# Kernel optimization log

Measured on AMD Instinct MI355X. Metric: run time of the kernel, lower is better.

## Reference

```python
import jax, jax.numpy as jnp
import numpy as np

OUT_FEATURES = 11008
IN_FEATURES = 4096
GROUP_SIZE = 32
NUM_GROUPS = OUT_FEATURES * IN_FEATURES // GROUP_SIZE        # 1,409,024
NUM_PACKED = NUM_GROUPS * (GROUP_SIZE // 8 * 3)              # 16,908,288 bytes


def block_dequantize_3bit(weight_q3, weight_norm):
    """Unpack 3-bit codes (8 values per 3 bytes) and dequantize to fp32."""
    p = weight_q3.reshape(-1, 3).astype(jnp.int32)  # [N/8, 3] bytes
    b0, b1, b2 = p[:, 0], p[:, 1], p[:, 2]
    q = jnp.stack([
        b0 & 7,
        (b0 >> 3) & 7,
        ((b0 >> 6) & 3) | ((b1 & 1) << 2),
        (b1 >> 1) & 7,
        (b1 >> 4) & 7,
        ((b1 >> 7) & 1) | ((b2 & 3) << 1),
        (b2 >> 2) & 7,
        (b2 >> 5) & 7,
    ], axis=-1)                                     # [N/8, 8] codes in 0..7
    q = q.reshape(NUM_GROUPS, GROUP_SIZE).astype(jnp.float32)
    norm = weight_norm.astype(jnp.float32)[:, None]  # [num_groups, 1]
    w = (q / 7.0) * 2.0 * norm - norm                # map [0,7] -> [-norm, norm]
    return w.reshape(OUT_FEATURES, IN_FEATURES)


def setup_inputs() -> dict:
    key = jax.random.key(0)
    k1, k2, k3, k4 = jax.random.split(key, 4)
    x = jax.random.normal(k1, (4, 128, IN_FEATURES), dtype=jnp.float32)
    weight_q3 = jax.random.randint(k2, (NUM_PACKED,), 0, 256, dtype=jnp.int32)
    weight_norm = (jax.random.uniform(k3, (NUM_GROUPS,), dtype=jnp.float32) * 0.1 + 0.01).astype(jnp.float16)
    bias = jax.random.normal(k4, (OUT_FEATURES,), dtype=jnp.float32) * 0.02
    return {"x": x, "weight_q3": weight_q3, "weight_norm": weight_norm, "bias": bias}


def reference(x, weight_q3, weight_norm, bias):
    w = block_dequantize_3bit(weight_q3, weight_norm)  # [out, in] fp32
    return jnp.einsum('bsd,od->bso', x, w) + bias
```

## Files before the change

kernel.cpp:

```cpp
#include <hip/hip_runtime.h>
#include <hip/hip_fp16.h>

#define M_TOTAL 512
#define N_TOTAL 11008
#define K_TOTAL 4096
#define BM 128
#define BN 64
#define BK 64
#define NT (K_TOTAL / BK)
#define LDK 72

typedef short bf16x8 __attribute__((ext_vector_type(8)));
typedef float f32x4 __attribute__((ext_vector_type(4)));

__device__ __forceinline__ unsigned int pack2_bf16(float f0, float f1) {
    unsigned int u0 = __builtin_bit_cast(unsigned int, f0) + 0x8000u;
    unsigned int u1 = __builtin_bit_cast(unsigned int, f1) + 0x8000u;
    return (u0 >> 16) | (u1 & 0xFFFF0000u);
}

__device__ __forceinline__ void async_ld16(void* lds, const void* g) {
    __builtin_amdgcn_global_load_lds(
        (const __attribute__((address_space(1))) unsigned int*)g,
        (__attribute__((address_space(3))) unsigned int*)lds, 16, 0, 0);
}

__device__ __forceinline__ int detect_mode_wave(const void* __restrict__ wn) {
    const int lane = threadIdx.x & 63;
    const unsigned short* u16 = (const unsigned short*)wn;
    const float* f32p = (const float*)wn;
    const float vb = __builtin_bit_cast(float, (unsigned int)u16[lane] << 16);
    const float vh = __half2float(__builtin_bit_cast(__half, u16[lane]));
    const float vf = f32p[lane];
    const unsigned long long mb = __ballot(vb > 0.005f && vb < 0.12f);
    const unsigned long long mh = __ballot(vh > 0.005f && vh < 0.12f);
    (void)vf;
    return (mb == ~0ull) ? 2 : ((mh == ~0ull) ? 1 : 0);
}

__global__ void __launch_bounds__(256)
convert_x_kernel(const float* __restrict__ x, unsigned short* __restrict__ xb) {
    const int i = (blockIdx.x * 256 + threadIdx.x) * 4;
    const float4 v = *(const float4*)&x[i];
    *(uint2*)&xb[i] = make_uint2(pack2_bf16(v.x, v.y), pack2_bf16(v.z, v.w));
}

__global__ void __launch_bounds__(512, 6)
l3b_gemm_pipe(const unsigned short* __restrict__ xb, const int* __restrict__ wq,
              const void* __restrict__ wnorm, const float* __restrict__ bias,
              float* __restrict__ out)
{
    __shared__ unsigned short As[2][BM * 64];
    __shared__ unsigned short Bs[2][BN * 64];

    const int tid  = threadIdx.x;
    const int mode = detect_mode_wave(wnorm);

    const int bid = blockIdx.x;
    const int w   = (bid & 7) * 86 + (bid >> 3);
    const int m0  = (w & 3) * BM;
    const int n0  = (w >> 2) * BN;

    const int wid  = tid >> 6;
    const int lane = tid & 63;
    const int quad = lane >> 4;
    const int lm   = lane & 15;
    const int wm   = (wid >> 1) * 32;
    const int wn_  = (wid & 1) * 32;

    const int arow0 = wid * 8 + (lane >> 3);
    const int acol  = ((lane & 7) ^ ((lane >> 3) & 7)) * 8;
    const int aslot = (lane & 7) * 8;

    const int gl   = tid >> 2;
    const int sub  = tid & 3;
    const int bn_l = gl >> 1;
    const int kg   = gl & 1;
    const int ldsB = (bn_l << 6) + ((((kg * 4 + sub)) ^ (bn_l & 7)) << 3);

    auto stageA = [&](int it, int buf) {
#pragma unroll
        for (int j = 0; j < 2; ++j) {
            const int row = arow0 + j * 64;
            async_ld16(&As[buf][(row << 6) + aslot],
                       &xb[(size_t)(m0 + row) * K_TOTAL + it * 64 + acol]);
        }
    };

    auto loadNorm = [&](int g) -> float {
        if (mode == 0)      return ((const float*)wnorm)[g];
        else if (mode == 1) return __half2float(((const __half*)wnorm)[g]);
        else                return __builtin_bit_cast(float,
                               (unsigned int)((const unsigned short*)wnorm)[g] << 16);
    };
    auto loadB = [&](int it, int& b0, int& b1, int& b2, float& nrm) {
        const int g    = (n0 + bn_l) * (K_TOTAL / 32) + it * 2 + kg;
        const int base = g * 12 + sub * 3;
        b0 = wq[base]; b1 = wq[base + 1]; b2 = wq[base + 2];
        nrm = loadNorm(g);
    };
    auto decodeB = [&](int b0, int b1, int b2, float nrm, int buf) {
        const float a = nrm * (2.0f / 7.0f);
        const float b = -nrm;
        const unsigned int bits =
            (unsigned)b0 | ((unsigned)b1 << 8) | ((unsigned)b2 << 16);
        unsigned int packs[4];
#pragma unroll
        for (int j = 0; j < 4; ++j) {
            const float f0 = fmaf((float)((bits >> (6 * j)) & 7), a, b);
            const float f1 = fmaf((float)((bits >> (6 * j + 3)) & 7), a, b);
            packs[j] = pack2_bf16(f0, f1);
        }
        *(uint4*)&Bs[buf][ldsB] = make_uint4(packs[0], packs[1], packs[2], packs[3]);
    };

    f32x4 acc[2][2];
#pragma unroll
    for (int i = 0; i < 2; ++i)
#pragma unroll
        for (int j = 0; j < 2; ++j) acc[i][j] = (f32x4){0.f, 0.f, 0.f, 0.f};

    auto mfmaTile = [&](const unsigned short* Asb, const unsigned short* Bsb) {
#pragma unroll
        for (int ks = 0; ks < 2; ++ks) {
            const int cswz = (((ks * 4 + quad) ^ (lm & 7)) << 3);
            bf16x8 aF[2], bF[2];
#pragma unroll
            for (int mi = 0; mi < 2; ++mi)
                aF[mi] = *(const bf16x8*)&Asb[((wm + mi * 16 + lm) << 6) + cswz];
#pragma unroll
            for (int ni = 0; ni < 2; ++ni)
                bF[ni] = *(const bf16x8*)&Bsb[((wn_ + ni * 16 + lm) << 6) + cswz];
#pragma unroll
            for (int mi = 0; mi < 2; ++mi)
#pragma unroll
                for (int ni = 0; ni < 2; ++ni)
                    acc[mi][ni] = __builtin_amdgcn_mfma_f32_16x16x32_bf16(
                        aF[mi], bF[ni], acc[mi][ni], 0, 0, 0);
        }
    };

    int b0a, b1a, b2a; float na;
    int b0b, b1b, b2b; float nb;

    stageA(0, 0);
    loadB(0, b0a, b1a, b2a, na);
    decodeB(b0a, b1a, b2a, na, 0);
    loadB(1, b0b, b1b, b2b, nb);
    __syncthreads();

    for (int it = 0; it < NT; it += 2) {
        if (it + 1 < NT) stageA(it + 1, 1);
        if (it + 2 < NT) loadB(it + 2, b0a, b1a, b2a, na);
        if (it + 1 < NT) decodeB(b0b, b1b, b2b, nb, 1);
        mfmaTile(As[0], Bs[0]);
        __syncthreads();

        if (it + 2 < NT) stageA(it + 2, 0);
        if (it + 3 < NT) loadB(it + 3, b0b, b1b, b2b, nb);
        if (it + 2 < NT) decodeB(b0a, b1a, b2a, na, 0);
        mfmaTile(As[1], Bs[1]);
        __syncthreads();
    }

#pragma unroll
    for (int ni = 0; ni < 2; ++ni) {
        const int o  = n0 + wn_ + ni * 16 + lm;
        const float bv = bias[o];
#pragma unroll
        for (int mi = 0; mi < 2; ++mi) {
#pragma unroll
            for (int r = 0; r < 4; ++r) {
                const int m = m0 + wm + mi * 16 + quad * 4 + r;
                out[m * N_TOTAL + o] = acc[mi][ni][r] + bv;
            }
        }
    }
}

__global__ void __launch_bounds__(256)
l3b_gemm_kernel(const float* __restrict__ x, const int* __restrict__ wq,
                const void* __restrict__ wnorm, const float* __restrict__ bias,
                float* __restrict__ out)
{
    __shared__ unsigned short As[128 * LDK];
    __shared__ unsigned short Bs[64 * LDK];

    const int mode = detect_mode_wave(wnorm);
    const int tid  = threadIdx.x;
    const int m0   = blockIdx.y * 128;
    const int n0   = blockIdx.x * 64;
    const int wid  = tid >> 6;
    const int lane = tid & 63;
    const int quad = lane >> 4;
    const int lm   = lane & 15;
    const int wm   = (wid >> 1) * 64;
    const int wn   = (wid & 1) * 32;

    f32x4 acc[4][2];
#pragma unroll
    for (int i = 0; i < 4; ++i)
#pragma unroll
        for (int j = 0; j < 2; ++j) acc[i][j] = (f32x4){0.f, 0.f, 0.f, 0.f};

    const int ar = tid >> 4;
    const int ac = (tid & 15) * 4;
    const int gin      = tid >> 1;
    const int half     = tid & 1;
    const int bn_local = gin >> 1;
    const int bkg      = gin & 1;

    for (int it = 0; it < NT; ++it) {
        const int k0 = it * BK;
        __syncthreads();
#pragma unroll
        for (int p = 0; p < 8; ++p) {
            const int row = p * 16 + ar;
            const float4 v = *(const float4*)&x[(m0 + row) * K_TOTAL + k0 + ac];
            *(uint2*)&As[row * LDK + ac] =
                make_uint2(pack2_bf16(v.x, v.y), pack2_bf16(v.z, v.w));
        }
        {
            const int g    = (n0 + bn_local) * (K_TOTAL / 32) + it * 2 + bkg;
            const int base = g * 12 + half * 6;
            const int2 w0 = *(const int2*)&wq[base];
            const int2 w1 = *(const int2*)&wq[base + 2];
            const int2 w2 = *(const int2*)&wq[base + 4];
            float nrm;
            if (mode == 0)      nrm = ((const float*)wnorm)[g];
            else if (mode == 1) nrm = __half2float(((const __half*)wnorm)[g]);
            else                nrm = __builtin_bit_cast(float,
                                    (unsigned int)((const unsigned short*)wnorm)[g] << 16);
            const float a = nrm * (2.0f / 7.0f);
            const float b = -nrm;
            const unsigned int bits0 =
                (unsigned)w0.x | ((unsigned)w0.y << 8) | ((unsigned)w1.x << 16);
            const unsigned int bits1 =
                (unsigned)w1.y | ((unsigned)w2.x << 8) | ((unsigned)w2.y << 16);
            unsigned int packs[8];
#pragma unroll
            for (int t3 = 0; t3 < 2; ++t3) {
                const unsigned int bits = t3 ? bits1 : bits0;
#pragma unroll
                for (int j = 0; j < 4; ++j) {
                    const float f0 = fmaf((float)((bits >> (6 * j)) & 7), a, b);
                    const float f1 = fmaf((float)((bits >> (6 * j + 3)) & 7), a, b);
                    packs[t3 * 4 + j] = pack2_bf16(f0, f1);
                }
            }
            unsigned int* dst = (unsigned int*)&Bs[bn_local * LDK + bkg * 32 + half * 16];
            *(uint4*)dst       = make_uint4(packs[0], packs[1], packs[2], packs[3]);
            *(uint4*)(dst + 4) = make_uint4(packs[4], packs[5], packs[6], packs[7]);
        }
        __syncthreads();
#pragma unroll
        for (int ks = 0; ks < 2; ++ks) {
            const int kb = ks * 32 + quad * 8;
            bf16x8 aF[4], bF[2];
#pragma unroll
            for (int mi = 0; mi < 4; ++mi)
                aF[mi] = *(const bf16x8*)&As[(wm + mi * 16 + lm) * LDK + kb];
#pragma unroll
            for (int ni = 0; ni < 2; ++ni)
                bF[ni] = *(const bf16x8*)&Bs[(wn + ni * 16 + lm) * LDK + kb];
#pragma unroll
            for (int mi = 0; mi < 4; ++mi)
#pragma unroll
                for (int ni = 0; ni < 2; ++ni)
                    acc[mi][ni] = __builtin_amdgcn_mfma_f32_16x16x32_bf16(
                        aF[mi], bF[ni], acc[mi][ni], 0, 0, 0);
        }
    }
#pragma unroll
    for (int ni = 0; ni < 2; ++ni) {
        const int o  = n0 + wn + ni * 16 + lm;
        const float bv = bias[o];
#pragma unroll
        for (int mi = 0; mi < 4; ++mi)
#pragma unroll
            for (int r = 0; r < 4; ++r) {
                const int m = m0 + wm + mi * 16 + quad * 4 + r;
                out[m * N_TOTAL + o] = acc[mi][ni][r] + bv;
            }
    }
}

extern "C" void kernel_launch(void* const* d_in, const int* in_sizes, int n_in,
                              void* d_out, int out_size, void* d_ws, size_t ws_size,
                              hipStream_t stream) {
    const float* x    = (const float*)d_in[0];
    const int*   wq   = (const int*)d_in[1];
    const void*  wn   = d_in[2];
    const float* bias = (const float*)d_in[3];
    float* out = (float*)d_out;

    const size_t need = 256 + (size_t)M_TOTAL * K_TOTAL * 2;
    if (ws_size >= need) {
        unsigned short* xb = (unsigned short*)((char*)d_ws + 256);
        convert_x_kernel<<<(M_TOTAL * K_TOTAL / 4) / 256, 256, 0, stream>>>(x, xb);
        l3b_gemm_pipe<<<(M_TOTAL / BM) * (N_TOTAL / BN), 512, 0, stream>>>(
            xb, wq, wn, bias, out);
    } else {
        dim3 grid(N_TOTAL / 64, M_TOTAL / 128);
        l3b_gemm_kernel<<<grid, 256, 0, stream>>>(x, wq, wn, bias, out);
    }
}
```

Measured before the change: 200.5 us.

## Halve threads per block and give each wave a larger 64x32 output tile

Cuts the GEMM block from 512 to 256 threads and doubles each wave's M tile to four 16-row MFMA fragments, so each B fragment read from LDS is reused across more A fragments. Each thread now loads and decodes twice as many packed weight words, using int2 loads, and writes two 16-byte LDS chunks. Memory-level parallelism per block and occupancy drop, while register pressure rises from the larger accumulator array.

```diff
diff --git a/kernel.cpp b/kernel.cpp
--- a/kernel.cpp
+++ b/kernel.cpp
@@ -45,7 +45,7 @@
     *(uint2*)&xb[i] = make_uint2(pack2_bf16(v.x, v.y), pack2_bf16(v.z, v.w));
 }
 
-__global__ void __launch_bounds__(512, 6)
+__global__ void __launch_bounds__(256, 3)
 l3b_gemm_pipe(const unsigned short* __restrict__ xb, const int* __restrict__ wq,
               const void* __restrict__ wnorm, const float* __restrict__ bias,
               float* __restrict__ out)
@@ -65,23 +65,26 @@
     const int lane = tid & 63;
     const int quad = lane >> 4;
     const int lm   = lane & 15;
-    const int wm   = (wid >> 1) * 32;
+    const int wm   = (wid >> 1) * 64;
     const int wn_  = (wid & 1) * 32;
 
     const int arow0 = wid * 8 + (lane >> 3);
     const int acol  = ((lane & 7) ^ ((lane >> 3) & 7)) * 8;
     const int aslot = (lane & 7) * 8;
 
-    const int gl   = tid >> 2;
-    const int sub  = tid & 3;
+    const int gl   = tid >> 1;
+    const int hf   = tid & 1;
     const int bn_l = gl >> 1;
     const int kg   = gl & 1;
-    const int ldsB = (bn_l << 6) + ((((kg * 4 + sub)) ^ (bn_l & 7)) << 3);
+    const int sw   = bn_l & 7;
+    const int c0   = kg * 4 + hf * 2;
+    const int ldsB0 = (bn_l << 6) + (((c0    ) ^ sw) << 3);
+    const int ldsB1 = (bn_l << 6) + (((c0 + 1) ^ sw) << 3);
 
     auto stageA = [&](int it, int buf) {
 #pragma unroll
-        for (int j = 0; j < 2; ++j) {
-            const int row = arow0 + j * 64;
+        for (int j = 0; j < 4; ++j) {
+            const int row = arow0 + j * 32;
             async_ld16(&As[buf][(row << 6) + aslot],
                        &xb[(size_t)(m0 + row) * K_TOTAL + it * 64 + acol]);
         }
@@ -93,30 +96,39 @@
         else                return __builtin_bit_cast(float,
                                (unsigned int)((const unsigned short*)wnorm)[g] << 16);
     };
-    auto loadB = [&](int it, int& b0, int& b1, int& b2, float& nrm) {
+    auto loadB = [&](int it, int2& w0, int2& w1, int2& w2, float& nrm) {
         const int g    = (n0 + bn_l) * (K_TOTAL / 32) + it * 2 + kg;
-        const int base = g * 12 + sub * 3;
-        b0 = wq[base]; b1 = wq[base + 1]; b2 = wq[base + 2];
+        const int base = g * 12 + hf * 6;
+        w0 = *(const int2*)&wq[base];
+        w1 = *(const int2*)&wq[base + 2];
+        w2 = *(const int2*)&wq[base + 4];
         nrm = loadNorm(g);
     };
-    auto decodeB = [&](int b0, int b1, int b2, float nrm, int buf) {
+    auto decodeB = [&](int2 w0, int2 w1, int2 w2, float nrm, int buf) {
         const float a = nrm * (2.0f / 7.0f);
         const float b = -nrm;
-        const unsigned int bits =
-            (unsigned)b0 | ((unsigned)b1 << 8) | ((unsigned)b2 << 16);
-        unsigned int packs[4];
-#pragma unroll
-        for (int j = 0; j < 4; ++j) {
-            const float f0 = fmaf((float)((bits >> (6 * j)) & 7), a, b);
-            const float f1 = fmaf((float)((bits >> (6 * j + 3)) & 7), a, b);
-            packs[j] = pack2_bf16(f0, f1);
-        }
-        *(uint4*)&Bs[buf][ldsB] = make_uint4(packs[0], packs[1], packs[2], packs[3]);
-    };
-
-    f32x4 acc[2][2];
-#pragma unroll
-    for (int i = 0; i < 2; ++i)
+        const unsigned int bits0 =
+            (unsigned)w0.x | ((unsigned)w0.y << 8) | ((unsigned)w1.x << 16);
+        const unsigned int bits1 =
+            (unsigned)w1.y | ((unsigned)w2.x << 8) | ((unsigned)w2.y << 16);
+        unsigned int packs[8];
+#pragma unroll
+        for (int t3 = 0; t3 < 2; ++t3) {
+            const unsigned int bits = t3 ? bits1 : bits0;
+#pragma unroll
+            for (int j = 0; j < 4; ++j) {
+                const float f0 = fmaf((float)((bits >> (6 * j)) & 7), a, b);
+                const float f1 = fmaf((float)((bits >> (6 * j + 3)) & 7), a, b);
+                packs[t3 * 4 + j] = pack2_bf16(f0, f1);
+            }
+        }
+        *(uint4*)&Bs[buf][ldsB0] = make_uint4(packs[0], packs[1], packs[2], packs[3]);
+        *(uint4*)&Bs[buf][ldsB1] = make_uint4(packs[4], packs[5], packs[6], packs[7]);
+    };
+
+    f32x4 acc[4][2];
+#pragma unroll
+    for (int i = 0; i < 4; ++i)
 #pragma unroll
         for (int j = 0; j < 2; ++j) acc[i][j] = (f32x4){0.f, 0.f, 0.f, 0.f};
 
@@ -124,15 +136,15 @@
 #pragma unroll
         for (int ks = 0; ks < 2; ++ks) {
             const int cswz = (((ks * 4 + quad) ^ (lm & 7)) << 3);
-            bf16x8 aF[2], bF[2];
-#pragma unroll
-            for (int mi = 0; mi < 2; ++mi)
+            bf16x8 aF[4], bF[2];
+#pragma unroll
+            for (int mi = 0; mi < 4; ++mi)
                 aF[mi] = *(const bf16x8*)&Asb[((wm + mi * 16 + lm) << 6) + cswz];
 #pragma unroll
             for (int ni = 0; ni < 2; ++ni)
                 bF[ni] = *(const bf16x8*)&Bsb[((wn_ + ni * 16 + lm) << 6) + cswz];
 #pragma unroll
-            for (int mi = 0; mi < 2; ++mi)
+            for (int mi = 0; mi < 4; ++mi)
 #pragma unroll
                 for (int ni = 0; ni < 2; ++ni)
                     acc[mi][ni] = __builtin_amdgcn_mfma_f32_16x16x32_bf16(
@@ -140,25 +152,25 @@
         }
     };
 
-    int b0a, b1a, b2a; float na;
-    int b0b, b1b, b2b; float nb;
+    int2 w0a, w1a, w2a; float na;
+    int2 w0b, w1b, w2b; float nb;
 
     stageA(0, 0);
-    loadB(0, b0a, b1a, b2a, na);
-    decodeB(b0a, b1a, b2a, na, 0);
-    loadB(1, b0b, b1b, b2b, nb);
+    loadB(0, w0a, w1a, w2a, na);
+    decodeB(w0a, w1a, w2a, na, 0);
+    loadB(1, w0b, w1b, w2b, nb);
     __syncthreads();
 
     for (int it = 0; it < NT; it += 2) {
         if (it + 1 < NT) stageA(it + 1, 1);
-        if (it + 2 < NT) loadB(it + 2, b0a, b1a, b2a, na);
-        if (it + 1 < NT) decodeB(b0b, b1b, b2b, nb, 1);
+        if (it + 2 < NT) loadB(it + 2, w0a, w1a, w2a, na);
+        if (it + 1 < NT) decodeB(w0b, w1b, w2b, nb, 1);
         mfmaTile(As[0], Bs[0]);
         __syncthreads();
 
         if (it + 2 < NT) stageA(it + 2, 0);
-        if (it + 3 < NT) loadB(it + 3, b0b, b1b, b2b, nb);
-        if (it + 2 < NT) decodeB(b0a, b1a, b2a, na, 0);
+        if (it + 3 < NT) loadB(it + 3, w0b, w1b, w2b, nb);
+        if (it + 2 < NT) decodeB(w0a, w1a, w2a, na, 0);
         mfmaTile(As[1], Bs[1]);
         __syncthreads();
     }
@@ -168,7 +180,7 @@
         const int o  = n0 + wn_ + ni * 16 + lm;
         const float bv = bias[o];
 #pragma unroll
-        for (int mi = 0; mi < 2; ++mi) {
+        for (int mi = 0; mi < 4; ++mi) {
 #pragma unroll
             for (int r = 0; r < 4; ++r) {
                 const int m = m0 + wm + mi * 16 + quad * 4 + r;
@@ -298,7 +310,7 @@
     if (ws_size >= need) {
         unsigned short* xb = (unsigned short*)((char*)d_ws + 256);
         convert_x_kernel<<<(M_TOTAL * K_TOTAL / 4) / 256, 256, 0, stream>>>(x, xb);
-        l3b_gemm_pipe<<<(M_TOTAL / BM) * (N_TOTAL / BN), 512, 0, stream>>>(
+        l3b_gemm_pipe<<<(M_TOTAL / BM) * (N_TOTAL / BN), 256, 0, stream>>>(
             xb, wq, wn, bias, out);
     } else {
         dim3 grid(N_TOTAL / 64, M_TOTAL / 128);
```

Measured after the change: 198.6 us. No clear change (-0.9%).
